# Performance work log

Hardware: AMD Instinct MI355X
Metric: run time of the kernel (lower is better)

The kernel has to match this reference:

```python
import jax, jax.numpy as jnp
import numpy as np

N = 8192
MARGIN = 0.2
LAMB = 0.012
ITERS = 5


def setup_inputs() -> dict:
    key = jax.random.key(0)
    # sims in [0,1): cosine-similarity-like scores; exp(-(1-s)/lamb) needs s near [0,1]
    sims = jax.random.uniform(key, (N, N), dtype=jnp.float32)
    return {"sims": sims}


def _ot(sims):
    # Sinkhorn-Knopp normalization, r = c = ones so (r/u) == 1/u, (c/v) == 1/v
    P = jnp.exp(-(1.0 - sims) / LAMB)
    P = P / jnp.sum(P)  # global normalization (dims [-2,-1])
    for _ in range(ITERS):
        u = P.sum(axis=-1, keepdims=True)   # row sums  [N,1]
        P = P / u
        v = P.sum(axis=-2, keepdims=True)   # col sums  [1,N]
        P = P / v
    return P


def reference(sims):
    P = _ot(sims)
    d = jnp.diagonal(P)                     # [N]
    eye = jnp.eye(P.shape[0], dtype=bool)
    # cost_im: anchor = column diagonal (d[j]); cost_s: anchor = row diagonal (d[i])
    cost_im = jnp.where(eye, 0.0, jnp.maximum(P - d[None, :] + MARGIN, 0.0))
    cost_s = jnp.where(eye, 0.0, jnp.maximum(P - d[:, None] + MARGIN, 0.0))
    # max_violation = False -> sum over all hinge terms
    return cost_s.sum() + cost_im.sum()
```

## Files before the change

### kernel.cpp

```cpp
#include <hip/hip_runtime.h>


#define NN 8192u
#define MARGIN 0.2f
#define KF (1.4426950408889634f / 0.012f)

__device__ __forceinline__ float blk_reduce(float v, float* red) {
#pragma unroll
  for (int off = 32; off; off >>= 1) v += __shfl_down(v, off, 64);
  const int lane = threadIdx.x & 63, wid = threadIdx.x >> 6;
  __syncthreads();
  if (lane == 0) red[wid] = v;
  __syncthreads();
  return red[0] + red[1] + red[2] + red[3];
}

__device__ __forceinline__ void unpk4(uint q, float& f0, float& f1, float& f2,
                                      float& f3) {
  auto lo = __builtin_amdgcn_cvt_pk_f32_fp8((int)q, false);
  auto hi = __builtin_amdgcn_cvt_pk_f32_fp8((int)q, true);
  f0 = lo[0]; f1 = lo[1]; f2 = hi[0]; f3 = hi[1];
}

template <bool USEQ>
__global__ __launch_bounds__(256) void k_pass0(const float* __restrict__ sims,
                                               uint* __restrict__ Qw,
                                               float* __restrict__ R) {
  __shared__ float red[4];
  const uint row = blockIdx.x;
  const uint t = threadIdx.x;
  float acc = 0.f;
#pragma unroll
  for (uint ch = 0; ch < 8; ++ch) {
    const uint col = ch * 1024u + t * 4u;
    const float4 s = *(const float4*)(sims + row * NN + col);
    const float p0 = exp2f((s.x - 1.f) * KF);
    const float p1 = exp2f((s.y - 1.f) * KF);
    const float p2 = exp2f((s.z - 1.f) * KF);
    const float p3 = exp2f((s.w - 1.f) * KF);
    if constexpr (USEQ) {
      int pk = 0;
      pk = __builtin_amdgcn_cvt_pk_fp8_f32(p0, p1, pk, false);
      pk = __builtin_amdgcn_cvt_pk_fp8_f32(p2, p3, pk, true);
      Qw[(row * NN + col) >> 2] = (uint)pk;
      float q0, q1, q2, q3;
      unpk4((uint)pk, q0, q1, q2, q3);
      acc += (q0 + q1) + (q2 + q3);
    } else {
      acc += (p0 + p1) + (p2 + p3);
    }
  }
  const float s = blk_reduce(acc, red);
  if (t == 0) R[row] = 1.f / s;
}

template <bool USEQ>
__global__ __launch_bounds__(256) void k_colmv(const float* __restrict__ sims,
                                               const uint* __restrict__ Qw,
                                               const float* __restrict__ R,
                                               float* __restrict__ part) {
  const uint t = threadIdx.x;
  const uint col = blockIdx.x * 1024u + t * 4u;
  const uint row0 = blockIdx.y * 128u;
  float a0 = 0.f, a1 = 0.f, a2 = 0.f, a3 = 0.f;
  for (uint rr = 0; rr < 128u; ++rr) {
    const uint row = row0 + rr;
    const float Rr = R[row];
    if constexpr (USEQ) {
      float f0, f1, f2, f3;
      unpk4(Qw[(row * NN + col) >> 2], f0, f1, f2, f3);
      a0 += f0 * Rr; a1 += f1 * Rr; a2 += f2 * Rr; a3 += f3 * Rr;
    } else {
      const float4 s = *(const float4*)(sims + row * NN + col);
      a0 += exp2f((s.x - 1.f) * KF) * Rr;
      a1 += exp2f((s.y - 1.f) * KF) * Rr;
      a2 += exp2f((s.z - 1.f) * KF) * Rr;
      a3 += exp2f((s.w - 1.f) * KF) * Rr;
    }
  }
  float4 o; o.x = a0; o.y = a1; o.z = a2; o.w = a3;
  *(float4*)(part + blockIdx.y * NN + col) = o;
}

template <bool USEQ>
__global__ __launch_bounds__(256) void k_colred(const float* __restrict__ part,
                                                float* __restrict__ Cg, int fin,
                                                const float* __restrict__ sims,
                                                const uint* __restrict__ Qw,
                                                const float* __restrict__ R,
                                                float* __restrict__ dvec,
                                                float* __restrict__ out) {
  const uint j = blockIdx.x * 256u + threadIdx.x;
  float s = 0.f;
#pragma unroll 8
  for (uint r = 0; r < 64u; ++r) s += part[r * NN + j];
  const float c = 1.f / s;
  Cg[j] = c;
  if (fin) {
    float pd;
    if constexpr (USEQ) {
      const uint u = Qw[(j * 8193u) >> 2];
      const uint b = (u >> ((j & 3u) * 8u)) & 0xFFu;
      pd = __builtin_amdgcn_cvt_f32_fp8((int)b, 0);
    } else {
      pd = exp2f((sims[j * 8193u] - 1.f) * KF);
    }
    dvec[j] = pd * R[j] * c;
    if (j == 0) *out = 0.f;
  }
}

template <bool USEQ>
__global__ __launch_bounds__(256) void k_rowmv(const float* __restrict__ sims,
                                               const uint* __restrict__ Qw,
                                               const float* __restrict__ Cg,
                                               float* __restrict__ R) {
  __shared__ float ldsC[NN];
  __shared__ float red[4];
  const uint t = threadIdx.x;
  for (uint c = t * 4u; c < NN; c += 1024u)
    *(float4*)(ldsC + c) = *(const float4*)(Cg + c);
  __syncthreads();
#pragma unroll
  for (uint r = 0; r < 4u; ++r) {
    const uint row = blockIdx.x * 4u + r;
    float acc = 0.f;
#pragma unroll
    for (uint ch = 0; ch < 2u; ++ch) {
      const uint col = ch * 4096u + t * 16u;
      const float4 c0 = *(const float4*)(ldsC + col);
      const float4 c1 = *(const float4*)(ldsC + col + 4);
      const float4 c2 = *(const float4*)(ldsC + col + 8);
      const float4 c3 = *(const float4*)(ldsC + col + 12);
      if constexpr (USEQ) {
        const uint4 q = *(const uint4*)(Qw + row * 2048u + (col >> 2));
        float a0, a1, a2, a3, b0, b1, b2, b3;
        unpk4(q.x, a0, a1, a2, a3);
        unpk4(q.y, b0, b1, b2, b3);
        acc += a0 * c0.x + a1 * c0.y + a2 * c0.z + a3 * c0.w;
        acc += b0 * c1.x + b1 * c1.y + b2 * c1.z + b3 * c1.w;
        unpk4(q.z, a0, a1, a2, a3);
        unpk4(q.w, b0, b1, b2, b3);
        acc += a0 * c2.x + a1 * c2.y + a2 * c2.z + a3 * c2.w;
        acc += b0 * c3.x + b1 * c3.y + b2 * c3.z + b3 * c3.w;
      } else {
        const float* sp = sims + row * NN + col;
        const float4 s0 = *(const float4*)(sp);
        const float4 s1 = *(const float4*)(sp + 4);
        const float4 s2 = *(const float4*)(sp + 8);
        const float4 s3 = *(const float4*)(sp + 12);
        acc += exp2f((s0.x - 1.f) * KF) * c0.x + exp2f((s0.y - 1.f) * KF) * c0.y +
               exp2f((s0.z - 1.f) * KF) * c0.z + exp2f((s0.w - 1.f) * KF) * c0.w;
        acc += exp2f((s1.x - 1.f) * KF) * c1.x + exp2f((s1.y - 1.f) * KF) * c1.y +
               exp2f((s1.z - 1.f) * KF) * c1.z + exp2f((s1.w - 1.f) * KF) * c1.w;
        acc += exp2f((s2.x - 1.f) * KF) * c2.x + exp2f((s2.y - 1.f) * KF) * c2.y +
               exp2f((s2.z - 1.f) * KF) * c2.z + exp2f((s2.w - 1.f) * KF) * c2.w;
        acc += exp2f((s3.x - 1.f) * KF) * c3.x + exp2f((s3.y - 1.f) * KF) * c3.y +
               exp2f((s3.z - 1.f) * KF) * c3.z + exp2f((s3.w - 1.f) * KF) * c3.w;
      }
    }
    const float s = blk_reduce(acc, red);
    if (t == 0) R[row] = 1.f / s;
  }
}

template <bool USEQ>
__global__ __launch_bounds__(256) void k_loss(const float* __restrict__ sims,
                                              const uint* __restrict__ Qw,
                                              const float* __restrict__ R,
                                              const float* __restrict__ Cg,
                                              const float* __restrict__ dvec,
                                              float* __restrict__ out) {
  __shared__ float red[4];
  const uint t = threadIdx.x;
  const uint col = blockIdx.x * 1024u + t * 4u;
  const uint row0 = blockIdx.y * 128u;
  const float4 c4 = *(const float4*)(Cg + col);
  const float4 d4 = *(const float4*)(dvec + col);
  float acc = 0.f;
  for (uint rr = 0; rr < 128u; ++rr) {
    const uint row = row0 + rr;
    const float Rr = R[row];
    const float dr = dvec[row];
    float f0, f1, f2, f3;
    if constexpr (USEQ) {
      unpk4(Qw[(row * NN + col) >> 2], f0, f1, f2, f3);
    } else {
      const float4 s = *(const float4*)(sims + row * NN + col);
      f0 = exp2f((s.x - 1.f) * KF);
      f1 = exp2f((s.y - 1.f) * KF);
      f2 = exp2f((s.z - 1.f) * KF);
      f3 = exp2f((s.w - 1.f) * KF);
    }
    float p, h;
    p = f0 * Rr * c4.x;
    h = fmaxf(p - d4.x + MARGIN, 0.f) + fmaxf(p - dr + MARGIN, 0.f);
    acc += (row == col + 0u) ? 0.f : h;
    p = f1 * Rr * c4.y;
    h = fmaxf(p - d4.y + MARGIN, 0.f) + fmaxf(p - dr + MARGIN, 0.f);
    acc += (row == col + 1u) ? 0.f : h;
    p = f2 * Rr * c4.z;
    h = fmaxf(p - d4.z + MARGIN, 0.f) + fmaxf(p - dr + MARGIN, 0.f);
    acc += (row == col + 2u) ? 0.f : h;
    p = f3 * Rr * c4.w;
    h = fmaxf(p - d4.w + MARGIN, 0.f) + fmaxf(p - dr + MARGIN, 0.f);
    acc += (row == col + 3u) ? 0.f : h;
  }
  const float s = blk_reduce(acc, red);
  if (t == 0) atomicAdd(out, s);
}

template <bool USEQ>
static void run_all(const float* sims, float* out, void* ws, hipStream_t stream) {
  uint* Qw;
  float* R;
  if (USEQ) {
    Qw = (uint*)ws;
    R = (float*)((char*)ws + (size_t)NN * NN);
  } else {
    Qw = nullptr;
    R = (float*)ws;
  }
  float* C = R + NN;
  float* dv = C + NN;
  float* part = dv + NN;

  k_pass0<USEQ><<<8192, 256, 0, stream>>>(sims, Qw, R);
  for (int it = 0; it < 5; ++it) {
    k_colmv<USEQ><<<dim3(8, 64), 256, 0, stream>>>(sims, Qw, R, part);
    k_colred<USEQ><<<32, 256, 0, stream>>>(part, C, (it == 4) ? 1 : 0, sims, Qw,
                                           R, dv, out);
    if (it < 4) k_rowmv<USEQ><<<2048, 256, 0, stream>>>(sims, Qw, C, R);
  }
  k_loss<USEQ><<<dim3(8, 64), 256, 0, stream>>>(sims, Qw, R, C, dv, out);
}

extern "C" void kernel_launch(void* const* d_in, const int* in_sizes, int n_in,
                              void* d_out, int out_size, void* d_ws,
                              size_t ws_size, hipStream_t stream) {
  const float* sims = (const float*)d_in[0];
  float* out = (float*)d_out;
  const size_t need_q =
      (size_t)NN * NN + (size_t)(3 * NN + 64 * NN) * sizeof(float);
  if (ws_size >= need_q) {
    run_all<true>(sims, out, d_ws, stream);
  } else {
    run_all<false>(sims, out, d_ws, stream);
  }
}
```

Baseline: 538.1 us.

## Replace column partial-reduce kernel with atomics and fold reciprocals into consumers

The separate column-reduction kernel is removed. Each column-sum block now atomically accumulates into a double-buffered column-sum vector, and the next pass zeroes the other buffer. Reciprocals of the column sums are computed where they are consumed (rowmv LDS load, loss kernel), the diagonal of the quantized matrix is captured during the first pass, and the rowmv kernel now handles 8 rows per block. Fast hardware exp2 and rcp intrinsics replace the library calls, and the non-quantized fallback is dropped. This cuts launch count and partial-buffer traffic, at the cost of nondeterministic float atomics and reliance on a large enough workspace.

```diff
diff --git a/kernel.cpp b/kernel.cpp
--- a/kernel.cpp
+++ b/kernel.cpp
@@ -4,6 +4,16 @@
 #define NN 8192u
 #define MARGIN 0.2f
 #define KF (1.4426950408889634f / 0.012f)
+
+__device__ __forceinline__ float fexp2(float x) { return __builtin_amdgcn_exp2f(x); }
+__device__ __forceinline__ float frcp(float x) { return __builtin_amdgcn_rcpf(x); }
+
+__device__ __forceinline__ void unpk4(uint q, float& f0, float& f1, float& f2,
+                                      float& f3) {
+  auto lo = __builtin_amdgcn_cvt_pk_f32_fp8((int)q, false);
+  auto hi = __builtin_amdgcn_cvt_pk_f32_fp8((int)q, true);
+  f0 = lo[0]; f1 = lo[1]; f2 = hi[0]; f3 = hi[1];
+}
 
 __device__ __forceinline__ float blk_reduce(float v, float* red) {
 #pragma unroll
@@ -15,17 +25,12 @@
   return red[0] + red[1] + red[2] + red[3];
 }
 
-__device__ __forceinline__ void unpk4(uint q, float& f0, float& f1, float& f2,
-                                      float& f3) {
-  auto lo = __builtin_amdgcn_cvt_pk_f32_fp8((int)q, false);
-  auto hi = __builtin_amdgcn_cvt_pk_f32_fp8((int)q, true);
-  f0 = lo[0]; f1 = lo[1]; f2 = hi[0]; f3 = hi[1];
-}
-
-template <bool USEQ>
 __global__ __launch_bounds__(256) void k_pass0(const float* __restrict__ sims,
                                                uint* __restrict__ Qw,
-                                               float* __restrict__ R) {
+                                               float* __restrict__ R,
+                                               float* __restrict__ Qd,
+                                               float* __restrict__ Cs0,
+                                               float* __restrict__ out) {
   __shared__ float red[4];
   const uint row = blockIdx.x;
   const uint t = threadIdx.x;
@@ -33,97 +38,74 @@
 #pragma unroll
   for (uint ch = 0; ch < 8; ++ch) {
     const uint col = ch * 1024u + t * 4u;
-    const float4 s = *(const float4*)(sims + row * NN + col);
-    const float p0 = exp2f((s.x - 1.f) * KF);
-    const float p1 = exp2f((s.y - 1.f) * KF);
-    const float p2 = exp2f((s.z - 1.f) * KF);
-    const float p3 = exp2f((s.w - 1.f) * KF);
-    if constexpr (USEQ) {
-      int pk = 0;
-      pk = __builtin_amdgcn_cvt_pk_fp8_f32(p0, p1, pk, false);
-      pk = __builtin_amdgcn_cvt_pk_fp8_f32(p2, p3, pk, true);
-      Qw[(row * NN + col) >> 2] = (uint)pk;
-      float q0, q1, q2, q3;
-      unpk4((uint)pk, q0, q1, q2, q3);
-      acc += (q0 + q1) + (q2 + q3);
-    } else {
-      acc += (p0 + p1) + (p2 + p3);
+    const float4 s = *(const float4*)(sims + (size_t)row * NN + col);
+    const float p0 = fexp2((s.x - 1.f) * KF);
+    const float p1 = fexp2((s.y - 1.f) * KF);
+    const float p2 = fexp2((s.z - 1.f) * KF);
+    const float p3 = fexp2((s.w - 1.f) * KF);
+    int pk = 0;
+    pk = __builtin_amdgcn_cvt_pk_fp8_f32(p0, p1, pk, false);
+    pk = __builtin_amdgcn_cvt_pk_fp8_f32(p2, p3, pk, true);
+    Qw[((size_t)row * NN + col) >> 2] = (uint)pk;
+    float q0, q1, q2, q3;
+    unpk4((uint)pk, q0, q1, q2, q3);
+    acc += (q0 + q1) + (q2 + q3);
+    if (col == (row & ~3u)) {
+      const uint sel = row & 3u;
+      Qd[row] = sel == 0u ? q0 : sel == 1u ? q1 : sel == 2u ? q2 : q3;
     }
   }
   const float s = blk_reduce(acc, red);
-  if (t == 0) R[row] = 1.f / s;
+  if (t == 0) R[row] = frcp(s);
+  if (row < 32u) Cs0[row * 256u + t] = 0.f;
+  if (row == 0 && t == 0) *out = 0.f;
 }
 
-template <bool USEQ>
-__global__ __launch_bounds__(256) void k_colmv(const float* __restrict__ sims,
-                                               const uint* __restrict__ Qw,
+__global__ __launch_bounds__(256) void k_colmv(const uint* __restrict__ Qw,
                                                const float* __restrict__ R,
-                                               float* __restrict__ part) {
+                                               float* __restrict__ dst,
+                                               float* __restrict__ zero_other) {
   const uint t = threadIdx.x;
   const uint col = blockIdx.x * 1024u + t * 4u;
   const uint row0 = blockIdx.y * 128u;
+  if (blockIdx.y == 0u) {
+    float4 z; z.x = z.y = z.z = z.w = 0.f;
+    *(float4*)(zero_other + col) = z;
+  }
   float a0 = 0.f, a1 = 0.f, a2 = 0.f, a3 = 0.f;
+  const uint* qp = Qw + (((size_t)row0 * NN + col) >> 2);
+#pragma unroll 4
   for (uint rr = 0; rr < 128u; ++rr) {
-    const uint row = row0 + rr;
-    const float Rr = R[row];
-    if constexpr (USEQ) {
-      float f0, f1, f2, f3;
-      unpk4(Qw[(row * NN + col) >> 2], f0, f1, f2, f3);
-      a0 += f0 * Rr; a1 += f1 * Rr; a2 += f2 * Rr; a3 += f3 * Rr;
-    } else {
-      const float4 s = *(const float4*)(sims + row * NN + col);
-      a0 += exp2f((s.x - 1.f) * KF) * Rr;
-      a1 += exp2f((s.y - 1.f) * KF) * Rr;
-      a2 += exp2f((s.z - 1.f) * KF) * Rr;
-      a3 += exp2f((s.w - 1.f) * KF) * Rr;
-    }
+    const float Rr = R[row0 + rr];
+    float f0, f1, f2, f3;
+    unpk4(qp[rr * 2048u], f0, f1, f2, f3);
+    a0 = fmaf(f0, Rr, a0);
+    a1 = fmaf(f1, Rr, a1);
+    a2 = fmaf(f2, Rr, a2);
+    a3 = fmaf(f3, Rr, a3);
   }
-  float4 o; o.x = a0; o.y = a1; o.z = a2; o.w = a3;
-  *(float4*)(part + blockIdx.y * NN + col) = o;
+  atomicAdd(dst + col + 0, a0);
+  atomicAdd(dst + col + 1, a1);
+  atomicAdd(dst + col + 2, a2);
+  atomicAdd(dst + col + 3, a3);
 }
 
-template <bool USEQ>
-__global__ __launch_bounds__(256) void k_colred(const float* __restrict__ part,
-                                                float* __restrict__ Cg, int fin,
-                                                const float* __restrict__ sims,
-                                                const uint* __restrict__ Qw,
-                                                const float* __restrict__ R,
-                                                float* __restrict__ dvec,
-                                                float* __restrict__ out) {
-  const uint j = blockIdx.x * 256u + threadIdx.x;
-  float s = 0.f;
-#pragma unroll 8
-  for (uint r = 0; r < 64u; ++r) s += part[r * NN + j];
-  const float c = 1.f / s;
-  Cg[j] = c;
-  if (fin) {
-    float pd;
-    if constexpr (USEQ) {
-      const uint u = Qw[(j * 8193u) >> 2];
-      const uint b = (u >> ((j & 3u) * 8u)) & 0xFFu;
-      pd = __builtin_amdgcn_cvt_f32_fp8((int)b, 0);
-    } else {
-      pd = exp2f((sims[j * 8193u] - 1.f) * KF);
-    }
-    dvec[j] = pd * R[j] * c;
-    if (j == 0) *out = 0.f;
-  }
-}
-
-template <bool USEQ>
-__global__ __launch_bounds__(256) void k_rowmv(const float* __restrict__ sims,
-                                               const uint* __restrict__ Qw,
-                                               const float* __restrict__ Cg,
+__global__ __launch_bounds__(256) void k_rowmv(const uint* __restrict__ Qw,
+                                               const float* __restrict__ Csrc,
                                                float* __restrict__ R) {
   __shared__ float ldsC[NN];
   __shared__ float red[4];
   const uint t = threadIdx.x;
-  for (uint c = t * 4u; c < NN; c += 1024u)
-    *(float4*)(ldsC + c) = *(const float4*)(Cg + c);
+  for (uint c = t * 4u; c < NN; c += 1024u) {
+    const float4 s = *(const float4*)(Csrc + c);
+    float4 o;
+    o.x = frcp(s.x); o.y = frcp(s.y); o.z = frcp(s.z); o.w = frcp(s.w);
+    *(float4*)(ldsC + c) = o;
+  }
   __syncthreads();
 #pragma unroll
-  for (uint r = 0; r < 4u; ++r) {
-    const uint row = blockIdx.x * 4u + r;
+  for (uint r = 0; r < 8u; ++r) {
+    const uint row = blockIdx.x * 8u + r;
     float acc = 0.f;
 #pragma unroll
     for (uint ch = 0; ch < 2u; ++ch) {
@@ -132,107 +114,64 @@
       const float4 c1 = *(const float4*)(ldsC + col + 4);
       const float4 c2 = *(const float4*)(ldsC + col + 8);
       const float4 c3 = *(const float4*)(ldsC + col + 12);
-      if constexpr (USEQ) {
-        const uint4 q = *(const uint4*)(Qw + row * 2048u + (col >> 2));
-        float a0, a1, a2, a3, b0, b1, b2, b3;
-        unpk4(q.x, a0, a1, a2, a3);
-        unpk4(q.y, b0, b1, b2, b3);
-        acc += a0 * c0.x + a1 * c0.y + a2 * c0.z + a3 * c0.w;
-        acc += b0 * c1.x + b1 * c1.y + b2 * c1.z + b3 * c1.w;
-        unpk4(q.z, a0, a1, a2, a3);
-        unpk4(q.w, b0, b1, b2, b3);
-        acc += a0 * c2.x + a1 * c2.y + a2 * c2.z + a3 * c2.w;
-        acc += b0 * c3.x + b1 * c3.y + b2 * c3.z + b3 * c3.w;
-      } else {
-        const float* sp = sims + row * NN + col;
-        const float4 s0 = *(const float4*)(sp);
-        const float4 s1 = *(const float4*)(sp + 4);
-        const float4 s2 = *(const float4*)(sp + 8);
-        const float4 s3 = *(const float4*)(sp + 12);
-        acc += exp2f((s0.x - 1.f) * KF) * c0.x + exp2f((s0.y - 1.f) * KF) * c0.y +
-               exp2f((s0.z - 1.f) * KF) * c0.z + exp2f((s0.w - 1.f) * KF) * c0.w;
-        acc += exp2f((s1.x - 1.f) * KF) * c1.x + exp2f((s1.y - 1.f) * KF) * c1.y +
-               exp2f((s1.z - 1.f) * KF) * c1.z + exp2f((s1.w - 1.f) * KF) * c1.w;
-        acc += exp2f((s2.x - 1.f) * KF) * c2.x + exp2f((s2.y - 1.f) * KF) * c2.y +
-               exp2f((s2.z - 1.f) * KF) * c2.z + exp2f((s2.w - 1.f) * KF) * c2.w;
-        acc += exp2f((s3.x - 1.f) * KF) * c3.x + exp2f((s3.y - 1.f) * KF) * c3.y +
-               exp2f((s3.z - 1.f) * KF) * c3.z + exp2f((s3.w - 1.f) * KF) * c3.w;
-      }
+      const uint4 q = *(const uint4*)(Qw + (size_t)row * 2048u + (col >> 2));
+      float a0, a1, a2, a3, b0, b1, b2, b3;
+      unpk4(q.x, a0, a1, a2, a3);
+      unpk4(q.y, b0, b1, b2, b3);
+      acc += a0 * c0.x + a1 * c0.y + a2 * c0.z + a3 * c0.w;
+      acc += b0 * c1.x + b1 * c1.y + b2 * c1.z + b3 * c1.w;
+      unpk4(q.z, a0, a1, a2, a3);
+      unpk4(q.w, b0, b1, b2, b3);
+      acc += a0 * c2.x + a1 * c2.y + a2 * c2.z + a3 * c2.w;
+      acc += b0 * c3.x + b1 * c3.y + b2 * c3.z + b3 * c3.w;
     }
     const float s = blk_reduce(acc, red);
-    if (t == 0) R[row] = 1.f / s;
+    if (t == 0) R[row] = frcp(s);
   }
 }
 
-template <bool USEQ>
-__global__ __launch_bounds__(256) void k_loss(const float* __restrict__ sims,
-                                              const uint* __restrict__ Qw,
+__global__ __launch_bounds__(256) void k_loss(const uint* __restrict__ Qw,
                                               const float* __restrict__ R,
-                                              const float* __restrict__ Cg,
-                                              const float* __restrict__ dvec,
+                                              const float* __restrict__ Cs,
+                                              const float* __restrict__ Qd,
                                               float* __restrict__ out) {
   __shared__ float red[4];
   const uint t = threadIdx.x;
   const uint col = blockIdx.x * 1024u + t * 4u;
   const uint row0 = blockIdx.y * 128u;
-  const float4 c4 = *(const float4*)(Cg + col);
-  const float4 d4 = *(const float4*)(dvec + col);
+  const float4 cs4 = *(const float4*)(Cs + col);
+  const float4 r4 = *(const float4*)(R + col);
+  const float4 qd4 = *(const float4*)(Qd + col);
+  const float ci0 = frcp(cs4.x), ci1 = frcp(cs4.y), ci2 = frcp(cs4.z),
+              ci3 = frcp(cs4.w);
+  const float d0 = qd4.x * r4.x * ci0;
+  const float d1 = qd4.y * r4.y * ci1;
+  const float d2 = qd4.z * r4.z * ci2;
+  const float d3 = qd4.w * r4.w * ci3;
   float acc = 0.f;
+  const uint* qp = Qw + (((size_t)row0 * NN + col) >> 2);
   for (uint rr = 0; rr < 128u; ++rr) {
     const uint row = row0 + rr;
     const float Rr = R[row];
-    const float dr = dvec[row];
+    const float dr = Qd[row] * Rr * frcp(Cs[row]);
     float f0, f1, f2, f3;
-    if constexpr (USEQ) {
-      unpk4(Qw[(row * NN + col) >> 2], f0, f1, f2, f3);
-    } else {
-      const float4 s = *(const float4*)(sims + row * NN + col);
-      f0 = exp2f((s.x - 1.f) * KF);
-      f1 = exp2f((s.y - 1.f) * KF);
-      f2 = exp2f((s.z - 1.f) * KF);
-      f3 = exp2f((s.w - 1.f) * KF);
-    }
+    unpk4(qp[rr * 2048u], f0, f1, f2, f3);
     float p, h;
-    p = f0 * Rr * c4.x;
-    h = fmaxf(p - d4.x + MARGIN, 0.f) + fmaxf(p - dr + MARGIN, 0.f);
+    p = f0 * Rr * ci0;
+    h = fmaxf(p - d0 + MARGIN, 0.f) + fmaxf(p - dr + MARGIN, 0.f);
     acc += (row == col + 0u) ? 0.f : h;
-    p = f1 * Rr * c4.y;
-    h = fmaxf(p - d4.y + MARGIN, 0.f) + fmaxf(p - dr + MARGIN, 0.f);
+    p = f1 * Rr * ci1;
+    h = fmaxf(p - d1 + MARGIN, 0.f) + fmaxf(p - dr + MARGIN, 0.f);
     acc += (row == col + 1u) ? 0.f : h;
-    p = f2 * Rr * c4.z;
-    h = fmaxf(p - d4.z + MARGIN, 0.f) + fmaxf(p - dr + MARGIN, 0.f);
+    p = f2 * Rr * ci2;
+    h = fmaxf(p - d2 + MARGIN, 0.f) + fmaxf(p - dr + MARGIN, 0.f);
     acc += (row == col + 2u) ? 0.f : h;
-    p = f3 * Rr * c4.w;
-    h = fmaxf(p - d4.w + MARGIN, 0.f) + fmaxf(p - dr + MARGIN, 0.f);
+    p = f3 * Rr * ci3;
+    h = fmaxf(p - d3 + MARGIN, 0.f) + fmaxf(p - dr + MARGIN, 0.f);
     acc += (row == col + 3u) ? 0.f : h;
   }
   const float s = blk_reduce(acc, red);
   if (t == 0) atomicAdd(out, s);
-}
-
-template <bool USEQ>
-static void run_all(const float* sims, float* out, void* ws, hipStream_t stream) {
-  uint* Qw;
-  float* R;
-  if (USEQ) {
-    Qw = (uint*)ws;
-    R = (float*)((char*)ws + (size_t)NN * NN);
-  } else {
-    Qw = nullptr;
-    R = (float*)ws;
-  }
-  float* C = R + NN;
-  float* dv = C + NN;
-  float* part = dv + NN;
-
-  k_pass0<USEQ><<<8192, 256, 0, stream>>>(sims, Qw, R);
-  for (int it = 0; it < 5; ++it) {
-    k_colmv<USEQ><<<dim3(8, 64), 256, 0, stream>>>(sims, Qw, R, part);
-    k_colred<USEQ><<<32, 256, 0, stream>>>(part, C, (it == 4) ? 1 : 0, sims, Qw,
-                                           R, dv, out);
-    if (it < 4) k_rowmv<USEQ><<<2048, 256, 0, stream>>>(sims, Qw, C, R);
-  }
-  k_loss<USEQ><<<dim3(8, 64), 256, 0, stream>>>(sims, Qw, R, C, dv, out);
 }
 
 extern "C" void kernel_launch(void* const* d_in, const int* in_sizes, int n_in,
@@ -240,11 +179,16 @@
                               size_t ws_size, hipStream_t stream) {
   const float* sims = (const float*)d_in[0];
   float* out = (float*)d_out;
-  const size_t need_q =
-      (size_t)NN * NN + (size_t)(3 * NN + 64 * NN) * sizeof(float);
-  if (ws_size >= need_q) {
-    run_all<true>(sims, out, d_ws, stream);
-  } else {
-    run_all<false>(sims, out, d_ws, stream);
+  uint* Qw = (uint*)d_ws;
+  float* fb = (float*)((char*)d_ws + (size_t)NN * NN);
+  float* R = fb;
+  float* Cs[2] = {fb + NN, fb + 2 * NN};
+  float* Qd = fb + 3 * NN;
+
+  k_pass0<<<8192, 256, 0, stream>>>(sims, Qw, R, Qd, Cs[0], out);
+  for (int k = 0; k < 5; ++k) {
+    k_colmv<<<dim3(8, 64), 256, 0, stream>>>(Qw, R, Cs[k & 1], Cs[(k + 1) & 1]);
+    if (k < 4) k_rowmv<<<1024, 256, 0, stream>>>(Qw, Cs[k & 1], R);
   }
+  k_loss<<<dim3(8, 64), 256, 0, stream>>>(Qw, R, Cs[0], Qd, out);
 }
```

After: 563.7 us. 1.05x slower.
